# Optimization experiments

Measured on AMD Instinct MI355X. Metric: run time of the kernel, lower is better.

Reference implementation:

```python
import jax, jax.numpy as jnp
import numpy as np

B, C, H, W = 8, 256, 64, 64
E, D, K = 4, 4, 2
CR = C // 16  # CBAM channel-attention reduction ratio 16

def _conv(x, w, pad):
    return jax.lax.conv_general_dilated(
        x, w, (1, 1), [(pad, pad), (pad, pad)],
        dimension_numbers=('NCHW', 'OIHW', 'NCHW'))

def _bn(x, s, b):  # eval-mode BatchNorm folded into per-channel affine
    return x * s[None, :, None, None] + b[None, :, None, None]

def _expert(p, x, dom_ids):
    # domain_transform: conv3x3-BN-GELU-conv3x3-BN
    h = jax.nn.gelu(_bn(_conv(x, p['dt_w1'], 1), p['dt_bn1s'], p['dt_bn1b']))
    d = _bn(_conv(h, p['dt_w2'], 1), p['dt_bn2s'], p['dt_bn2b'])
    # domain_gate: GAP -> conv1x1 C->1 -> sigmoid
    g1 = jax.nn.sigmoid(jnp.mean(d, (2, 3)) @ p['gate_w'] + p['gate_b'])  # [B]
    out = x + g1[:, None, None, None] * d
    # Res_CBAM_block (in==out channels, stride 1 -> identity shortcut)
    r = out
    h = jax.nn.relu(_bn(_conv(out, p['c1_w'], 1) + p['c1_b'][None, :, None, None], p['bn1s'], p['bn1b']))
    h = _bn(_conv(h, p['c2_w'], 1) + p['c2_b'][None, :, None, None], p['bn2s'], p['bn2b'])
    # channel attention (shared MLP over GAP and GMP)
    avg, mx = jnp.mean(h, (2, 3)), jnp.max(h, (2, 3))
    mlp = lambda v: jax.nn.relu(v @ p['ca_w1'].T) @ p['ca_w2'].T
    ca = jax.nn.sigmoid(mlp(avg) + mlp(mx))  # [B,C]
    h = h * ca[:, :, None, None]
    # spatial attention: 7x7 conv over [mean_c, max_c]
    sa_in = jnp.concatenate([jnp.mean(h, 1, keepdims=True), jnp.max(h, 1, keepdims=True)], axis=1)
    sa = jax.nn.sigmoid(_conv(sa_in, p['sa_w'], 3))
    h = jax.nn.relu(h * sa + r)
    # per-domain adapter bias (nn.Embedding lookup)
    return h + p['adp'][dom_ids][:, :, None, None]

def _forward(x, domain_ids, g_w1, g_b1, ln_s, ln_b, g_w2, g_b2, dom_emb,
             e_dt_w1, e_dt_bn1s, e_dt_bn1b, e_dt_w2, e_dt_bn2s, e_dt_bn2b,
             e_gate_w, e_gate_b, e_c1_w, e_c1_b, e_bn1s, e_bn1b,
             e_c2_w, e_c2_b, e_bn2s, e_bn2b, e_ca_w1, e_ca_w2, e_sa_w, e_adapter):
    ep = dict(dt_w1=e_dt_w1, dt_bn1s=e_dt_bn1s, dt_bn1b=e_dt_bn1b,
              dt_w2=e_dt_w2, dt_bn2s=e_dt_bn2s, dt_bn2b=e_dt_bn2b,
              gate_w=e_gate_w, gate_b=e_gate_b,
              c1_w=e_c1_w, c1_b=e_c1_b, bn1s=e_bn1s, bn1b=e_bn1b,
              c2_w=e_c2_w, c2_b=e_c2_b, bn2s=e_bn2s, bn2b=e_bn2b,
              ca_w1=e_ca_w1, ca_w2=e_ca_w2, sa_w=e_sa_w, adp=e_adapter)
    eouts = jax.vmap(_expert, in_axes=(0, None, None))(ep, x, domain_ids)  # [E,B,C,H,W]
    # gate input: [GAP(x) | GMP(x) | domain_embed(16)] -> Linear -> LN -> ReLU -> Linear -> softmax
    gi = jnp.concatenate([jnp.mean(x, (2, 3)), jnp.max(x, (2, 3)), dom_emb[domain_ids]], axis=1)
    hg = gi @ g_w1 + g_b1
    mu = jnp.mean(hg, -1, keepdims=True)
    var = jnp.var(hg, -1, keepdims=True)
    hg = jax.nn.relu((hg - mu) * jax.lax.rsqrt(var + 1e-5) * ln_s + ln_b)
    probs = jax.nn.softmax(hg @ g_w2 + g_b2, axis=-1)  # [B,E]
    vals, idx = jax.lax.top_k(probs, K)                # soft top-k routing
    wk = vals / jnp.sum(vals, -1, keepdims=True)       # renormalize top-k weights
    wfull = jnp.zeros_like(probs).at[jnp.arange(probs.shape[0])[:, None], idx].set(wk)
    return jnp.einsum('be,ebchw->bchw', wfull, eouts)

def setup_inputs():
    key = jax.random.key(0)
    ks = iter(jax.random.split(key, 48))
    rn = lambda shape, s=0.05: jax.random.normal(next(ks), shape, jnp.float32) * s
    p = {}
    p['x'] = jax.random.normal(next(ks), (B, C, H, W), jnp.float32)
    p['domain_ids'] = jax.random.randint(next(ks), (B,), 0, D)
    p['g_w1'] = rn((2 * C + 16, C)); p['g_b1'] = jnp.zeros((C,))
    p['ln_s'] = jnp.ones((C,)); p['ln_b'] = jnp.zeros((C,))
    p['g_w2'] = rn((C, E)); p['g_b2'] = jnp.zeros((E,))
    p['dom_emb'] = rn((D, 16), 0.5)
    p['e_dt_w1'] = rn((E, C, C, 3, 3)); p['e_dt_bn1s'] = jnp.ones((E, C)); p['e_dt_bn1b'] = jnp.zeros((E, C))
    p['e_dt_w2'] = rn((E, C, C, 3, 3)); p['e_dt_bn2s'] = jnp.ones((E, C)); p['e_dt_bn2b'] = jnp.zeros((E, C))
    p['e_gate_w'] = rn((E, C)); p['e_gate_b'] = jnp.zeros((E,))
    p['e_c1_w'] = rn((E, C, C, 3, 3)); p['e_c1_b'] = jnp.zeros((E, C))
    p['e_bn1s'] = jnp.ones((E, C)); p['e_bn1b'] = jnp.zeros((E, C))
    p['e_c2_w'] = rn((E, C, C, 3, 3)); p['e_c2_b'] = jnp.zeros((E, C))
    p['e_bn2s'] = jnp.ones((E, C)); p['e_bn2b'] = jnp.zeros((E, C))
    p['e_ca_w1'] = rn((E, CR, C)); p['e_ca_w2'] = rn((E, C, CR))
    p['e_sa_w'] = rn((E, 1, 2, 7, 7))
    p['e_adapter'] = rn((E, D, C), 0.1)
    return p

def reference(x, domain_ids, g_w1, g_b1, ln_s, ln_b, g_w2, g_b2, dom_emb,
              e_dt_w1, e_dt_bn1s, e_dt_bn1b, e_dt_w2, e_dt_bn2s, e_dt_bn2b,
              e_gate_w, e_gate_b, e_c1_w, e_c1_b, e_bn1s, e_bn1b,
              e_c2_w, e_c2_b, e_bn2s, e_bn2b, e_ca_w1, e_ca_w2, e_sa_w, e_adapter):
    return _forward(x, domain_ids, g_w1, g_b1, ln_s, ln_b, g_w2, g_b2, dom_emb,
                    e_dt_w1, e_dt_bn1s, e_dt_bn1b, e_dt_w2, e_dt_bn2s, e_dt_bn2b,
                    e_gate_w, e_gate_b, e_c1_w, e_c1_b, e_bn1s, e_bn1b,
                    e_c2_w, e_c2_b, e_bn2s, e_bn2b, e_ca_w1, e_ca_w2, e_sa_w, e_adapter)
```

## Files before the change

### kernel.cpp

```cpp
#include <hip/hip_runtime.h>
#include <math.h>

typedef __bf16 bf16x8 __attribute__((ext_vector_type(8)));
typedef __bf16 bf16x4 __attribute__((ext_vector_type(4)));
typedef float  f32x4  __attribute__((ext_vector_type(4)));

#define NB 8
#define NC 256
#define NHW 4096
#define NCHW_ 1048576
#define NSLOT 16

__device__ __forceinline__ float sigmoidf_(float x){ return 1.f/(1.f+expf(-x)); }
__device__ __forceinline__ float gelu_tanh(float x){
  float x3 = x*x*x;
  return 0.5f*x*(1.f+tanhf(0.7978845608028654f*(x + 0.044715f*x3)));
}

__device__ __forceinline__ void gload16(const void* g, void* l){
  __builtin_amdgcn_global_load_lds((const __attribute__((address_space(1))) void*)g,
                                   (__attribute__((address_space(3))) void*)l,
                                   16, 0, 0);
}

__global__ void k_prep_sb(const float* dt_bn1s, const float* dt_bn1b,
                          const float* dt_bn2s, const float* dt_bn2b,
                          const float* c1_b, const float* bn1s, const float* bn1b,
                          const float* c2_b, const float* bn2s, const float* bn2b,
                          float* effS, float* effB){
  int ec = blockIdx.x; int e = ec>>2, cv = ec&3; int c = threadIdx.x;
  int i = e*NC + c;
  float s, b;
  if (cv==0){ s = dt_bn1s[i]; b = dt_bn1b[i]; }
  else if (cv==1){ s = dt_bn2s[i]; b = dt_bn2b[i]; }
  else if (cv==2){ s = bn1s[i]; b = c1_b[i]*bn1s[i] + bn1b[i]; }
  else { s = bn2s[i]; b = c2_b[i]*bn2s[i] + bn2b[i]; }
  effS[ec*NC+c]=s; effB[ec*NC+c]=b;
}

__global__ void k_prep_w(const float* w0, const float* w1, const float* w2, const float* w3,
                         __bf16* wr){
  __shared__ float tl[9][257];
  int o = blockIdx.x; int ec = blockIdx.y; int e = ec>>2, cv = ec&3;
  int t = threadIdx.x;
  const float* src = (cv==0)?w0 : (cv==1)?w1 : (cv==2)?w2 : w3;
  const float* sp = src + ((size_t)((e*NC + o)*NC + t))*9;
  #pragma unroll
  for (int k=0;k<9;k++) tl[k][t] = sp[k];
  __syncthreads();
  __bf16* dst = wr + (size_t)ec*589824 + (size_t)o*256;
  #pragma unroll
  for (int k=0;k<9;k++) dst[(size_t)k*65536 + t] = (__bf16)tl[k][t];
}

__global__ void k_prep_x(const float* x, __bf16* xh, float* gps, float* gpm){
  __shared__ float tl[32][33];
  __shared__ float rs[256], rm[256];
  int ptile = blockIdx.x, p0 = ptile*32, c0 = blockIdx.y*32, b = blockIdx.z;
  int tx = threadIdx.x&31, ty = threadIdx.x>>5;
  #pragma unroll
  for (int k=0;k<4;k++){
    int c = c0 + ty + k*8;
    tl[ty+k*8][tx] = x[(size_t)(b*NC+c)*NHW + p0 + tx];
  }
  __syncthreads();
  #pragma unroll
  for (int k=0;k<4;k++){
    int p = p0 + ty + k*8;
    xh[(size_t)b*NCHW_ + (size_t)p*NC + c0 + tx] = (__bf16)tl[tx][ty+k*8];
  }
  int c_local = threadIdx.x & 31, seg = threadIdx.x >> 5;
  float s=0.f, m=-1e30f;
  #pragma unroll
  for (int j=0;j<4;j++){ float v = tl[c_local][seg*4+j]; s+=v; m=fmaxf(m,v); }
  rs[seg*32+c_local]=s; rm[seg*32+c_local]=m;
  __syncthreads();
  if (threadIdx.x < 32){
    float ss=0.f, mm=-1e30f;
    #pragma unroll
    for (int g=0; g<8; g++){ ss += rs[g*32+threadIdx.x]; mm = fmaxf(mm, rm[g*32+threadIdx.x]); }
    gps[(size_t)(b*128+ptile)*256 + c0 + threadIdx.x] = ss;
    gpm[(size_t)(b*128+ptile)*256 + c0 + threadIdx.x] = mm;
  }
}

__global__ void k_gate1b(const float* gps, const float* gpm, float* gavg, float* gmax){
  int b = blockIdx.x, c = threadIdx.x;
  float s=0.f, m=-1e30f;
  for (int k=0;k<128;k++){
    s += gps[(size_t)(b*128+k)*256 + c];
    m = fmaxf(m, gpm[(size_t)(b*128+k)*256 + c]);
  }
  gavg[b*256+c] = s/4096.f;
  gmax[b*256+c] = m;
}

__global__ void k_gate2(const float* gavg, const float* gmax, const int* dom,
                        const float* dom_emb, const float* w1, const float* b1,
                        const float* lns, const float* lnb,
                        const float* w2, const float* b2,
                        int* slot_e, float* slot_w){
  __shared__ float giT[528][8];
  __shared__ float hg[8][256];
  __shared__ float stat[16];
  __shared__ float logit[8][4];
  int t = threadIdx.x;
  for (int idx=t; idx<8*528; idx+=256){
    int b = idx&7, k = idx>>3;
    float v;
    if (k<256) v = gavg[b*256+k];
    else if (k<512) v = gmax[b*256+k-256];
    else v = dom_emb[dom[b]*16 + (k-512)];
    giT[k][b]=v;
  }
  __syncthreads();
  {
    float acc[8];
    float bb = b1[t];
    #pragma unroll
    for (int b=0;b<8;b++) acc[b]=bb;
    for (int k=0;k<528;k++){
      float wv = w1[k*256+t];
      #pragma unroll
      for (int b=0;b<8;b++) acc[b] += giT[k][b]*wv;
    }
    #pragma unroll
    for (int b=0;b<8;b++) hg[b][t]=acc[b];
  }
  __syncthreads();
  if (t<8){
    float mu=0.f; for(int c=0;c<256;c++) mu += hg[t][c]; mu/=256.f;
    float vr=0.f; for(int c=0;c<256;c++){ float d=hg[t][c]-mu; vr+=d*d; } vr/=256.f;
    stat[t]=mu; stat[8+t]=vr;
  }
  __syncthreads();
  for (int b=0;b<8;b++){
    float v = (hg[b][t]-stat[b])*rsqrtf(stat[8+b]+1e-5f)*lns[t]+lnb[t];
    hg[b][t] = fmaxf(v, 0.f);
  }
  __syncthreads();
  if (t<32){
    int b = t>>2, e = t&3;
    float acc = b2[e];
    for (int c=0;c<256;c++) acc += hg[b][c]*w2[c*4+e];
    logit[b][e]=acc;
  }
  __syncthreads();
  if (t==0){
    for (int b=0;b<8;b++){
      float mx = logit[b][0];
      for (int e=1;e<4;e++) mx = fmaxf(mx, logit[b][e]);
      float p[4], s=0.f;
      for (int e=0;e<4;e++){ p[e]=expf(logit[b][e]-mx); s+=p[e]; }
      for (int e=0;e<4;e++) p[e]/=s;
      int i0=0; for (int e=1;e<4;e++) if (p[e]>p[i0]) i0=e;
      int i1=-1; for (int e=0;e<4;e++){ if (e==i0) continue; if (i1<0 || p[e]>p[i1]) i1=e; }
      float den = p[i0]+p[i1];
      slot_e[2*b]   = i0; slot_w[2*b]   = p[i0]/den;
      slot_e[2*b+1] = i1; slot_w[2*b+1] = p[i1]/den;
    }
  }
}

template<int ACT, int RED>
__global__ __launch_bounds__(256,2) void k_conv(
    const __bf16* __restrict__ in0, int per_b,
    const __bf16* __restrict__ wr,  int conv_idx,
    const float* __restrict__ effS, const float* __restrict__ effB,
    const int* __restrict__ slot_e,
    const __bf16* __restrict__ zslab,
    __bf16* __restrict__ out,
    const float* __restrict__ gate_w, float* __restrict__ p_sum,
    float* __restrict__ ca_ps, float* __restrict__ ca_pm)
{
  __shared__ __bf16 smem[17408];
  __bf16* lA = smem;
  __bf16* lB = smem + 8192;

  const int tid   = threadIdx.x;
  const int lin   = blockIdx.y*64 + blockIdx.x;
  const int xcd   = lin & 7;
  const int q     = lin >> 3;
  const int slot  = (xcd<<1) | (q>>6);
  const int t64   = q & 63;
  const int tileM = t64 & 1;
  const int tileN = t64 >> 1;
  const int e     = slot_e[slot];
  const int cout_base = tileM*128;
  const int pos_base  = tileN*128;
  const int lane   = tid & 63;
  const int wv     = tid >> 6;
  const int lane15 = lane & 15, quad = lane >> 4;
  const int m_off  = (wv&1)*64, n_off = (wv>>1)*64;

  const __bf16* in = in0 + (size_t)(per_b ? (slot>>1) : slot) * NCHW_;
  const __bf16* wb = wr + (size_t)(e*4 + conv_idx) * 589824;

  int ldsOff[4];
  int aOff[4];
  int bBase[4];
  int rr0[4], cl0[4];
  #pragma unroll
  for (int j=0;j<4;j++){
    int f = (wv*4+j)*64 + lane;
    int row = f>>3, ph = f&7;
    int lc = ph ^ (row&7);
    ldsOff[j] = f*8;
    aOff[j]   = (cout_base + row)*256 + lc*8;
    int gp = pos_base + row;
    rr0[j] = gp>>6; cl0[j] = gp&63;
    bBase[j] = lc*8;
  }

  f32x4 zero = {0.f,0.f,0.f,0.f};
  f32x4 acc[4][4];
  #pragma unroll
  for (int i=0;i<4;i++)
    #pragma unroll
    for (int j=0;j<4;j++) acc[i][j] = zero;

  const int ph_read = lane15 & 7;

  for (int kk=0; kk<36; ++kk){
    const int k9 = kk>>2, c0e = (kk&3)*64;
    const int k3 = k9/3;
    const int dy = k3 - 1, dx = k9 - k3*3 - 1;
    __syncthreads();
    {
      const __bf16* ws = wb + (size_t)k9*65536 + c0e;
      #pragma unroll
      for (int j=0;j<4;j++)
        gload16(ws + aOff[j], lA + ldsOff[j]);
    }
    {
      const int doff = dy*16384 + dx*256 + c0e;
      #pragma unroll
      for (int j=0;j<4;j++){
        int rr = rr0[j] + dy, cl = cl0[j] + dx;
        const __bf16* src = ((unsigned)rr < 64u && (unsigned)cl < 64u)
            ? in + (size_t)(rr0[j]*16384 + cl0[j]*256 + doff + bBase[j])
            : zslab;
        gload16(src, lB + ldsOff[j]);
      }
    }
    __syncthreads();
    #pragma unroll
    for (int s=0;s<2;s++){
      bf16x8 af[4], bfr[4];
      const int ph = (s*4 + quad) ^ ph_read;
      #pragma unroll
      for (int i=0;i<4;i++) af[i]  = *(const bf16x8*)(lA + (m_off + i*16 + lane15)*64 + ph*8);
      #pragma unroll
      for (int j=0;j<4;j++) bfr[j] = *(const bf16x8*)(lB + (n_off + j*16 + lane15)*64 + ph*8);
      #pragma unroll
      for (int i=0;i<4;i++)
        #pragma unroll
        for (int j=0;j<4;j++)
          acc[i][j] = __builtin_amdgcn_mfma_f32_16x16x32_bf16(af[i], bfr[j], acc[i][j], 0,0,0);
    }
  }
  __syncthreads();

  const float* sS = effS + (e*4+conv_idx)*256 + cout_base;
  const float* sB = effB + (e*4+conv_idx)*256 + cout_base;
  float sc[16], bi[16];
  #pragma unroll
  for (int i=0;i<4;i++)
    #pragma unroll
    for (int r=0;r<4;r++){
      int m = m_off + i*16 + quad*4 + r;
      sc[i*4+r] = sS[m]; bi[i*4+r] = sB[m];
    }
  __bf16* lO = smem;
  #pragma unroll
  for (int i=0;i<4;i++){
    #pragma unroll
    for (int j=0;j<4;j++){
      int n = n_off + j*16 + lane15;
      #pragma unroll
      for (int r=0;r<4;r++){
        int m = m_off + i*16 + quad*4 + r;
        float v = acc[i][j][r]*sc[i*4+r] + bi[i*4+r];
        if (ACT==1) v = gelu_tanh(v);
        if (ACT==2) v = fmaxf(v, 0.f);
        lO[n*136 + m] = (__bf16)v;
      }
    }
  }
  __syncthreads();
  __bf16* ob = out + (size_t)slot*NCHW_;
  #pragma unroll
  for (int h=0; h<8; ++h){
    int chunk = tid + h*256;
    int prow = chunk>>4, part = chunk&15;
    *(uint4*)(ob + (size_t)(pos_base+prow)*256 + cout_base + part*8) =
      *(const uint4*)(lO + prow*136 + part*8);
  }

  if (RED==1){
    int m = tid & 127, half = tid >> 7;
    float s = 0.f;
    const __bf16* col = lO + (half*64)*136 + m;
    #pragma unroll 8
    for (int n=0;n<64;n++) s += (float)col[n*136];
    s *= gate_w[e*256 + cout_base + m];
    #pragma unroll
    for (int off=32; off; off>>=1) s += __shfl_down(s, off);
    __syncthreads();
    float* scr = (float*)smem;
    if (lane==0) scr[wv] = s;
    __syncthreads();
    if (tid==0) p_sum[slot*64 + tileN*2 + tileM] = scr[0]+scr[1]+scr[2]+scr[3];
  }
  if (RED==2){
    int m = tid & 127, half = tid >> 7;
    float s=0.f, mx=-1e30f;
    const __bf16* col = lO + (half*64)*136 + m;
    #pragma unroll 8
    for (int n=0;n<64;n++){ float v = (float)col[n*136]; s+=v; mx=fmaxf(mx,v); }
    __syncthreads();
    float* scr = (float*)smem;
    scr[half*128+m] = s; scr[256 + half*128+m] = mx;
    __syncthreads();
    if (tid<128){
      float ts = scr[tid] + scr[128+tid];
      float tm = fmaxf(scr[256+tid], scr[384+tid]);
      ca_ps[(size_t)(slot*32+tileN)*256 + cout_base + tid] = ts;
      ca_pm[(size_t)(slot*32+tileN)*256 + cout_base + tid] = tm;
    }
  }
}

__global__ void k_pw_r(const __bf16* xh, const __bf16* d, const float* p_sum,
                       const float* gate_b, const int* slot_e, __bf16* r){
  int slot = blockIdx.y;
  float tot = 0.f;
  #pragma unroll
  for (int k=0;k<64;k++) tot += p_sum[slot*64+k];
  float g1 = sigmoidf_(tot/4096.f + gate_b[slot_e[slot]]);
  size_t idx8 = ((size_t)blockIdx.x*256 + threadIdx.x)*8;
  bf16x8 xv = *(const bf16x8*)(xh + (size_t)(slot>>1)*NCHW_ + idx8);
  bf16x8 dv = *(const bf16x8*)(d + (size_t)slot*NCHW_ + idx8);
  bf16x8 rv;
  #pragma unroll
  for (int k=0;k<8;k++) rv[k] = (__bf16)((float)xv[k] + g1*(float)dv[k]);
  *(bf16x8*)(r + (size_t)slot*NCHW_ + idx8) = rv;
}

__global__ void k_ca2(const float* ps, const float* pm, const float* w1, const float* w2,
                      const int* slot_e, float* ca){
  __shared__ float avg[256], mxs[256], hr[32];
  int slot = blockIdx.x, t = threadIdx.x;
  int e = slot_e[slot];
  float s=0.f, m=-1e30f;
  #pragma unroll
  for (int k=0;k<32;k++){
    s += ps[(size_t)(slot*32+k)*256+t];
    m = fmaxf(m, pm[(size_t)(slot*32+k)*256+t]);
  }
  avg[t]=s/4096.f; mxs[t]=m;
  __syncthreads();
  if (t<32){
    int j = t&15; int which = t>>4;
    const float* v = which? mxs : avg;
    float acc=0.f;
    for (int c=0;c<256;c++) acc += v[c]*w1[e*4096 + j*256 + c];
    hr[t] = fmaxf(acc, 0.f);
  }
  __syncthreads();
  float acc=0.f;
  #pragma unroll
  for (int j=0;j<16;j++) acc += (hr[j]+hr[16+j])*w2[e*4096 + t*16 + j];
  ca[slot*256+t] = sigmoidf_(acc);
}

__global__ void k_sa1(const __bf16* h3, const float* ca, float* sam){
  int slot = blockIdx.y;
  int wv = threadIdx.x>>6, lane = threadIdx.x&63;
  int p = blockIdx.x*4 + wv;
  bf16x4 hv = *(const bf16x4*)(h3 + (size_t)slot*NCHW_ + (size_t)p*256 + lane*4);
  f32x4 cv = *(const f32x4*)(ca + slot*256 + lane*4);
  float s=0.f, m=-1e30f;
  #pragma unroll
  for (int k=0;k<4;k++){ float v = (float)hv[k]*cv[k]; s+=v; m=fmaxf(m,v); }
  #pragma unroll
  for (int off=32; off; off>>=1){ s += __shfl_down(s, off); m = fmaxf(m, __shfl_down(m, off)); }
  if (lane==0){ sam[slot*8192 + p] = s/256.f; sam[slot*8192 + 4096 + p] = m; }
}

__global__ void k_fin(const __bf16* h3, const __bf16* r, const float* ca, const float* sam,
                      const float* sa_w, const int* slot_e, const float* slot_w,
                      const float* adapter, const int* dom, float* out){
  __shared__ float tl[64][33];
  __shared__ float sAtt[2][32];
  const int p0 = blockIdx.x*32, c0 = blockIdx.y*64, b = blockIdx.z;
  const int t = threadIdx.x;
  const int s0 = b*2, s1 = s0+1;
  if (t < 64){
    int pp = p0 + (t&31);
    int sl = s0 + (t>>5);
    int e = slot_e[sl];
    int y = pp>>6, x0 = pp&63;
    const float* m0 = sam + sl*8192;
    const float* m1 = m0 + 4096;
    const float* w = sa_w + e*98;
    float acc = 0.f;
    for (int ky=0;ky<7;ky++){
      int yy = y+ky-3; if ((unsigned)yy>=64u) continue;
      for (int kx=0;kx<7;kx++){
        int xx = x0+kx-3; if ((unsigned)xx>=64u) continue;
        acc += w[ky*7+kx]*m0[yy*64+xx] + w[49+ky*7+kx]*m1[yy*64+xx];
      }
    }
    sAtt[t>>5][t&31] = sigmoidf_(acc);
  }
  __syncthreads();
  const int prow = t>>3;
  const int cchunk = t&7;
  const int pos = p0 + prow;
  const int cb = c0 + cchunk*8;
  const int e0 = slot_e[s0], e1 = slot_e[s1];
  const float w0 = slot_w[s0], w1 = slot_w[s1];
  const int dm = dom[b];
  size_t o0 = (size_t)s0*NCHW_ + (size_t)pos*256 + cb;
  size_t o1 = (size_t)s1*NCHW_ + (size_t)pos*256 + cb;
  bf16x8 h0v = *(const bf16x8*)(h3+o0), h1v = *(const bf16x8*)(h3+o1);
  bf16x8 r0v = *(const bf16x8*)(r+o0),  r1v = *(const bf16x8*)(r+o1);
  float sa0 = sAtt[0][prow], sa1 = sAtt[1][prow];
  #pragma unroll
  for (int k=0;k<8;k++){
    int c = cb + k;
    float v0 = (float)h0v[k]*ca[s0*256+c]*sa0 + (float)r0v[k];
    float v1 = (float)h1v[k]*ca[s1*256+c]*sa1 + (float)r1v[k];
    float val = w0*(fmaxf(v0,0.f) + adapter[(e0*4+dm)*256+c])
              + w1*(fmaxf(v1,0.f) + adapter[(e1*4+dm)*256+c]);
    tl[cchunk*8+k][prow] = val;
  }
  __syncthreads();
  const int cl = t>>2, px = (t&3)*8;
  #pragma unroll
  for (int k=0;k<8;k++)
    out[((size_t)(b*NC + c0 + cl))*NHW + p0 + px + k] = tl[cl][px+k];
}

extern "C" void kernel_launch(void* const* d_in, const int* in_sizes, int n_in,
                              void* d_out, int out_size, void* d_ws, size_t ws_size,
                              hipStream_t stream){
  const float* x      = (const float*)d_in[0];
  const int*   dom    = (const int*)d_in[1];
  const float* g_w1   = (const float*)d_in[2];
  const float* g_b1   = (const float*)d_in[3];
  const float* ln_s   = (const float*)d_in[4];
  const float* ln_b   = (const float*)d_in[5];
  const float* g_w2   = (const float*)d_in[6];
  const float* g_b2   = (const float*)d_in[7];
  const float* dom_emb= (const float*)d_in[8];
  const float* dt_w1  = (const float*)d_in[9];
  const float* dt_bn1s= (const float*)d_in[10];
  const float* dt_bn1b= (const float*)d_in[11];
  const float* dt_w2  = (const float*)d_in[12];
  const float* dt_bn2s= (const float*)d_in[13];
  const float* dt_bn2b= (const float*)d_in[14];
  const float* gate_w = (const float*)d_in[15];
  const float* gate_b = (const float*)d_in[16];
  const float* c1_w   = (const float*)d_in[17];
  const float* c1_b   = (const float*)d_in[18];
  const float* bn1s   = (const float*)d_in[19];
  const float* bn1b   = (const float*)d_in[20];
  const float* c2_w   = (const float*)d_in[21];
  const float* c2_b   = (const float*)d_in[22];
  const float* bn2s   = (const float*)d_in[23];
  const float* bn2b   = (const float*)d_in[24];
  const float* ca_w1  = (const float*)d_in[25];
  const float* ca_w2  = (const float*)d_in[26];
  const float* sa_w   = (const float*)d_in[27];
  const float* adapter= (const float*)d_in[28];

  char* ws = (char*)d_ws;
  size_t off = 0;
  auto alloc = [&](size_t bytes)->void*{
    void* p = ws + off; off += (bytes + 255) & ~size_t(255); return p;
  };
  __bf16* wr   = (__bf16*)alloc(16ull*589824*2);
  __bf16* xh   = (__bf16*)alloc(8ull*NCHW_*2);
  __bf16* bufA = (__bf16*)alloc(16ull*NCHW_*2);
  __bf16* bufB = (__bf16*)alloc(16ull*NCHW_*2);
  __bf16* bufC = (__bf16*)alloc(16ull*NCHW_*2);
  float* gps   = (float*)alloc(8ull*128*256*4);
  float* gpm   = (float*)alloc(8ull*128*256*4);
  float* gavg  = (float*)alloc(2048*4);
  float* gmax  = (float*)alloc(2048*4);
  float* effS  = (float*)alloc(4096*4);
  float* effB  = (float*)alloc(4096*4);
  int*   slot_e= (int*)alloc(64);
  float* slot_w= (float*)alloc(64);
  float* p_sum = (float*)alloc(16*64*4);
  float* ca_ps = (float*)alloc(16*32*256*4);
  float* ca_pm = (float*)alloc(16*32*256*4);
  float* ca    = (float*)alloc(16*256*4);
  float* sam   = (float*)alloc(16*8192*4);
  __bf16* zslab= (__bf16*)alloc(512);

  hipMemsetAsync(zslab, 0, 512, stream);

  k_prep_sb<<<dim3(16), dim3(256), 0, stream>>>(dt_bn1s, dt_bn1b, dt_bn2s, dt_bn2b,
                                                c1_b, bn1s, bn1b, c2_b, bn2s, bn2b, effS, effB);
  k_prep_w<<<dim3(256,16), dim3(256), 0, stream>>>(dt_w1, dt_w2, c1_w, c2_w, wr);
  k_prep_x<<<dim3(128,8,8), dim3(256), 0, stream>>>(x, xh, gps, gpm);
  k_gate1b<<<dim3(8), dim3(256), 0, stream>>>(gps, gpm, gavg, gmax);
  k_gate2<<<dim3(1), dim3(256), 0, stream>>>(gavg, gmax, dom, dom_emb, g_w1, g_b1,
                                             ln_s, ln_b, g_w2, g_b2, slot_e, slot_w);
  k_conv<1,0><<<dim3(64,16), dim3(256), 0, stream>>>(xh, 1, wr, 0, effS, effB, slot_e, zslab, bufA,
                                                     gate_w, p_sum, ca_ps, ca_pm);
  k_conv<0,1><<<dim3(64,16), dim3(256), 0, stream>>>(bufA, 0, wr, 1, effS, effB, slot_e, zslab, bufB,
                                                     gate_w, p_sum, ca_ps, ca_pm);
  k_pw_r<<<dim3(512,16), dim3(256), 0, stream>>>(xh, bufB, p_sum, gate_b, slot_e, bufC);
  k_conv<2,0><<<dim3(64,16), dim3(256), 0, stream>>>(bufC, 0, wr, 2, effS, effB, slot_e, zslab, bufA,
                                                     gate_w, p_sum, ca_ps, ca_pm);
  k_conv<0,2><<<dim3(64,16), dim3(256), 0, stream>>>(bufA, 0, wr, 3, effS, effB, slot_e, zslab, bufB,
                                                     gate_w, p_sum, ca_ps, ca_pm);
  k_ca2<<<dim3(16), dim3(256), 0, stream>>>(ca_ps, ca_pm, ca_w1, ca_w2, slot_e, ca);
  k_sa1<<<dim3(1024,16), dim3(256), 0, stream>>>(bufB, ca, sam);
  k_fin<<<dim3(128,4,8), dim3(256), 0, stream>>>(bufB, bufC, ca, sam, sa_w, slot_e, slot_w,
                                                 adapter, dom, (float*)d_out);
}
```

Baseline: 611.4 us.

## Fuse prep and gate-reduce kernels, raise conv occupancy bound to 4

Folds the BN scale/bias preparation into the weight-reformat kernel and folds the per-batch pooling reduction into the single-block gating kernel, removing two launches and two small buffers. Also raises the conv kernel's launch bounds minimum blocks per CU from 2 to 4 to encourage higher occupancy. The gating reduction now runs in one block instead of eight, serializing more memory reads. The tighter register budget may cause spills in the conv kernel.

```diff
diff --git a/kernel.cpp b/kernel.cpp
--- a/kernel.cpp
+++ b/kernel.cpp
@@ -23,26 +23,24 @@
                                    16, 0, 0);
 }
 
-__global__ void k_prep_sb(const float* dt_bn1s, const float* dt_bn1b,
-                          const float* dt_bn2s, const float* dt_bn2b,
-                          const float* c1_b, const float* bn1s, const float* bn1b,
-                          const float* c2_b, const float* bn2s, const float* bn2b,
-                          float* effS, float* effB){
-  int ec = blockIdx.x; int e = ec>>2, cv = ec&3; int c = threadIdx.x;
-  int i = e*NC + c;
-  float s, b;
-  if (cv==0){ s = dt_bn1s[i]; b = dt_bn1b[i]; }
-  else if (cv==1){ s = dt_bn2s[i]; b = dt_bn2b[i]; }
-  else if (cv==2){ s = bn1s[i]; b = c1_b[i]*bn1s[i] + bn1b[i]; }
-  else { s = bn2s[i]; b = c2_b[i]*bn2s[i] + bn2b[i]; }
-  effS[ec*NC+c]=s; effB[ec*NC+c]=b;
-}
-
 __global__ void k_prep_w(const float* w0, const float* w1, const float* w2, const float* w3,
-                         __bf16* wr){
+                         const float* dt_bn1s, const float* dt_bn1b,
+                         const float* dt_bn2s, const float* dt_bn2b,
+                         const float* c1_b, const float* bn1s, const float* bn1b,
+                         const float* c2_b, const float* bn2s, const float* bn2b,
+                         __bf16* wr, float* effS, float* effB){
   __shared__ float tl[9][257];
   int o = blockIdx.x; int ec = blockIdx.y; int e = ec>>2, cv = ec&3;
   int t = threadIdx.x;
+  if (o == 0){
+    int i = e*NC + t;
+    float s, b;
+    if (cv==0){ s = dt_bn1s[i]; b = dt_bn1b[i]; }
+    else if (cv==1){ s = dt_bn2s[i]; b = dt_bn2b[i]; }
+    else if (cv==2){ s = bn1s[i]; b = c1_b[i]*bn1s[i] + bn1b[i]; }
+    else { s = bn2s[i]; b = c2_b[i]*bn2s[i] + bn2b[i]; }
+    effS[ec*NC+t]=s; effB[ec*NC+t]=b;
+  }
   const float* src = (cv==0)?w0 : (cv==1)?w1 : (cv==2)?w2 : w3;
   const float* sp = src + ((size_t)((e*NC + o)*NC + t))*9;
   #pragma unroll
@@ -84,18 +82,7 @@
   }
 }
 
-__global__ void k_gate1b(const float* gps, const float* gpm, float* gavg, float* gmax){
-  int b = blockIdx.x, c = threadIdx.x;
-  float s=0.f, m=-1e30f;
-  for (int k=0;k<128;k++){
-    s += gps[(size_t)(b*128+k)*256 + c];
-    m = fmaxf(m, gpm[(size_t)(b*128+k)*256 + c]);
-  }
-  gavg[b*256+c] = s/4096.f;
-  gmax[b*256+c] = m;
-}
-
-__global__ void k_gate2(const float* gavg, const float* gmax, const int* dom,
+__global__ void k_gate2(const float* gps, const float* gpm, const int* dom,
                         const float* dom_emb, const float* w1, const float* b1,
                         const float* lns, const float* lnb,
                         const float* w2, const float* b2,
@@ -105,13 +92,18 @@
   __shared__ float stat[16];
   __shared__ float logit[8][4];
   int t = threadIdx.x;
-  for (int idx=t; idx<8*528; idx+=256){
-    int b = idx&7, k = idx>>3;
-    float v;
-    if (k<256) v = gavg[b*256+k];
-    else if (k<512) v = gmax[b*256+k-256];
-    else v = dom_emb[dom[b]*16 + (k-512)];
-    giT[k][b]=v;
+  for (int b=0;b<8;b++){
+    float s=0.f, m=-1e30f;
+    for (int k=0;k<128;k++){
+      s += gps[(size_t)(b*128+k)*256 + t];
+      m = fmaxf(m, gpm[(size_t)(b*128+k)*256 + t]);
+    }
+    giT[t][b]     = s/4096.f;
+    giT[256+t][b] = m;
+  }
+  if (t<16){
+    #pragma unroll
+    for (int b=0;b<8;b++) giT[512+t][b] = dom_emb[dom[b]*16 + t];
   }
   __syncthreads();
   {
@@ -163,7 +155,7 @@
 }
 
 template<int ACT, int RED>
-__global__ __launch_bounds__(256,2) void k_conv(
+__global__ __launch_bounds__(256,4) void k_conv(
     const __bf16* __restrict__ in0, int per_b,
     const __bf16* __restrict__ wr,  int conv_idx,
     const float* __restrict__ effS, const float* __restrict__ effB,
@@ -488,8 +480,6 @@
   __bf16* bufC = (__bf16*)alloc(16ull*NCHW_*2);
   float* gps   = (float*)alloc(8ull*128*256*4);
   float* gpm   = (float*)alloc(8ull*128*256*4);
-  float* gavg  = (float*)alloc(2048*4);
-  float* gmax  = (float*)alloc(2048*4);
   float* effS  = (float*)alloc(4096*4);
   float* effB  = (float*)alloc(4096*4);
   int*   slot_e= (int*)alloc(64);
@@ -503,12 +493,12 @@
 
   hipMemsetAsync(zslab, 0, 512, stream);
 
-  k_prep_sb<<<dim3(16), dim3(256), 0, stream>>>(dt_bn1s, dt_bn1b, dt_bn2s, dt_bn2b,
-                                                c1_b, bn1s, bn1b, c2_b, bn2s, bn2b, effS, effB);
-  k_prep_w<<<dim3(256,16), dim3(256), 0, stream>>>(dt_w1, dt_w2, c1_w, c2_w, wr);
+  k_prep_w<<<dim3(256,16), dim3(256), 0, stream>>>(dt_w1, dt_w2, c1_w, c2_w,
+                                                   dt_bn1s, dt_bn1b, dt_bn2s, dt_bn2b,
+                                                   c1_b, bn1s, bn1b, c2_b, bn2s, bn2b,
+                                                   wr, effS, effB);
   k_prep_x<<<dim3(128,8,8), dim3(256), 0, stream>>>(x, xh, gps, gpm);
-  k_gate1b<<<dim3(8), dim3(256), 0, stream>>>(gps, gpm, gavg, gmax);
-  k_gate2<<<dim3(1), dim3(256), 0, stream>>>(gavg, gmax, dom, dom_emb, g_w1, g_b1,
+  k_gate2<<<dim3(1), dim3(256), 0, stream>>>(gps, gpm, dom, dom_emb, g_w1, g_b1,
                                              ln_s, ln_b, g_w2, g_b2, slot_e, slot_w);
   k_conv<1,0><<<dim3(64,16), dim3(256), 0, stream>>>(xh, 1, wr, 0, effS, effB, slot_e, zslab, bufA,
                                                      gate_w, p_sum, ca_ps, ca_pm);
```

New measurement: 643.7 us. 1.05x slower.
